# Kernel tuning notes

Measured on AMD Instinct MI355X. Metric: run time of the kernel, lower is better.

## Reference

```python
import jax, jax.numpy as jnp
import numpy as np


def setup_inputs() -> dict:
    key = jax.random.key(0)
    ks = jax.random.split(key, 8)
    N, E, H, C, L, G = 100000, 1600000, 128, 10, 5, 64
    x = jax.random.normal(ks[0], (N, H), dtype=jnp.float32)
    edge_index = jax.random.randint(ks[1], (2, E), 0, N, dtype=jnp.int32)
    batch = jnp.sort(jax.random.randint(ks[2], (N,), 0, G, dtype=jnp.int32))
    # Glorot-ish init scale for stability
    Ws = jax.random.normal(ks[3], (L, H, H), dtype=jnp.float32) * (1.0 / np.sqrt(H))
    bs = jax.random.normal(ks[4], (L, H), dtype=jnp.float32) * 0.01
    W_out = jax.random.normal(ks[5], (H, C), dtype=jnp.float32) * (1.0 / np.sqrt(H))
    b_out = jax.random.normal(ks[6], (C,), dtype=jnp.float32) * 0.01
    return {"x": x, "edge_index": edge_index, "batch": batch, "num_graphs": G,
            "Ws": Ws, "bs": bs, "W_out": W_out, "b_out": b_out}


def reference(x, edge_index, batch, num_graphs, Ws, bs, W_out, b_out):
    N = x.shape[0]
    # --- GCN normalization (add self-loops, symmetric deg^-1/2 norm), computed once ---
    loop = jnp.arange(N, dtype=edge_index.dtype)
    src = jnp.concatenate([edge_index[0], loop])  # message sources (x_j)
    dst = jnp.concatenate([edge_index[1], loop])  # aggregation targets
    deg = jax.ops.segment_sum(jnp.ones_like(dst, dtype=x.dtype), dst, num_segments=N)
    dis = jnp.where(deg > 0, jax.lax.rsqrt(jnp.maximum(deg, 1.0)), 0.0)
    norm = dis[src] * dis[dst]  # [E+N]
    # --- stacked GCNConv + ReLU ---
    for l in range(Ws.shape[0]):
        xw = x @ Ws[l]                                   # [N, H] dense transform
        msg = norm[:, None] * xw[src]                    # gather + scale per edge
        x = jax.nn.relu(jax.ops.segment_sum(msg, dst, num_segments=N) + bs[l])
    # --- global mean pool over graphs ---
    sums = jax.ops.segment_sum(x, batch, num_segments=num_graphs)       # [G, H]
    cnts = jax.ops.segment_sum(jnp.ones((N,), x.dtype), batch, num_segments=num_graphs)
    pooled = sums / jnp.maximum(cnts, 1.0)[:, None]
    return pooled @ W_out + b_out
```

## Files before the change

kernel.cpp:

```cpp
#include <hip/hip_runtime.h>
#include <hip/hip_bf16.h>
#include <stdint.h>

#define HDIM 128
#define SBITS 8
#define SBMASK 255
#define SBMAX 512

typedef __attribute__((ext_vector_type(8))) short short8;
typedef __attribute__((ext_vector_type(4))) float f32x4;
typedef __attribute__((ext_vector_type(2))) float f32x2;

__device__ __forceinline__ ushort f2bf(float f) {
  uint u = __float_as_uint(f);
  u = (u + 0x7fffu + ((u >> 16) & 1u)) >> 16;
  return (ushort)u;
}
__device__ __forceinline__ float bflo(uint v) { return __uint_as_float(v << 16); }
__device__ __forceinline__ float bfhi(uint v) { return __uint_as_float(v & 0xffff0000u); }

__device__ __forceinline__ int pdeg4(int c) { return (c + 4) & ~3; }

__device__ __forceinline__ uint pack_cw(int src, float w) {
  uint w15 = (__float_as_uint(w) + 0x8000u) >> 16;
  return (uint)src | (w15 << 17);
}
__device__ __forceinline__ uint cw_src(uint u) { return u & 0x1FFFFu; }
__device__ __forceinline__ float cw_w(uint u) { return __uint_as_float((u >> 17) << 16); }


__global__ __launch_bounds__(256) void bucket_edges(const int* __restrict__ ei,
                                                    int* __restrict__ bktcur,
                                                    uint* __restrict__ bkt, int E,
                                                    int cap) {
  __shared__ int hist[SBMAX], base[SBMAX];
  const int t = threadIdx.x;
  const int c0 = blockIdx.x * 2048;
  for (int i = t; i < SBMAX; i += 256) hist[i] = 0;
  __syncthreads();
  uint pk[8];
  int sb_[8], rk[8];
#pragma unroll
  for (int j = 0; j < 8; ++j) {
    int idx = c0 + j * 256 + t;
    sb_[j] = -1;
    if (idx < E) {
      int s = ei[idx];
      int d = ei[E + idx];
      int b = d >> SBITS;
      pk[j] = (uint)(d & SBMASK) | ((uint)s << SBITS);
      sb_[j] = b;
      rk[j] = atomicAdd(&hist[b], 1);
    }
  }
  __syncthreads();
  for (int i = t; i < SBMAX; i += 256)
    base[i] = hist[i] ? atomicAdd(&bktcur[i * 16], hist[i]) : 0;
  __syncthreads();
#pragma unroll
  for (int j = 0; j < 8; ++j)
    if (sb_[j] >= 0)
      bkt[(size_t)sb_[j] * cap + base[sb_[j]] + rk[j]] = pk[j];
}

__global__ __launch_bounds__(256) void csr_count(const uint* __restrict__ bkt,
                                                 const int* __restrict__ bktcur,
                                                 float* __restrict__ dis,
                                                 int* __restrict__ degs,
                                                 int* __restrict__ sbtot, int cap,
                                                 int N) {
  __shared__ int cnt[256];
  __shared__ int red[256];
  const int sb = blockIdx.x, t = threadIdx.x;
  const int n0 = sb << SBITS;
  const int ecnt = bktcur[sb * 16];
  const uint* eb = bkt + (size_t)sb * cap;
  cnt[t] = 0;
  __syncthreads();
  for (int i = t; i < ecnt; i += 256)
    atomicAdd(&cnt[__builtin_nontemporal_load(eb + i) & SBMASK], 1);
  __syncthreads();
  int s = 0;
  const int n = n0 + t;
  if (n < N) {
    int c = cnt[t];
    degs[n] = c;
    dis[n] = rsqrtf((float)(c + 1));
    s = pdeg4(c);
  }
  red[t] = s;
  __syncthreads();
  for (int off = 128; off; off >>= 1) {
    if (t < off) red[t] += red[t + off];
    __syncthreads();
  }
  if (t == 0) sbtot[sb] = red[0];
}

__global__ __launch_bounds__(512) void scan_sb(const int* __restrict__ sbtot,
                                               int* __restrict__ sbbase,
                                               int* __restrict__ rowptr, int SB,
                                               int N) {
  __shared__ int sh[SBMAX];
  int t = threadIdx.x;
  int v = (t < SB) ? sbtot[t] : 0;
  sh[t] = v;
  __syncthreads();
  for (int off = 1; off < SBMAX; off <<= 1) {
    int add = (t >= off) ? sh[t - off] : 0;
    __syncthreads();
    sh[t] += add;
    __syncthreads();
  }
  if (t < SB) sbbase[t] = sh[t] - v;
  if (t == SBMAX - 1) rowptr[N] = sh[SBMAX - 1];
}

__global__ __launch_bounds__(256) void csr_place(const uint* __restrict__ bkt,
                                                 const int* __restrict__ bktcur,
                                                 const int* __restrict__ sbbase,
                                                 const float* __restrict__ dis,
                                                 const int* __restrict__ degs,
                                                 int* __restrict__ rowptr,
                                                 uint* __restrict__ colw, int cap,
                                                 int N) {
  __shared__ int cur[256];
  __shared__ int sh[256];
  const int sb = blockIdx.x, t = threadIdx.x;
  const int n0 = sb << SBITS;
  const int ecnt = bktcur[sb * 16];
  const uint* eb = bkt + (size_t)sb * cap;
  const int base = sbbase[sb];
  const int n = n0 + t;
  const int deg = (n < N) ? degs[n] : 0;
  const int v = (n < N) ? pdeg4(deg) : 0;
  sh[t] = v;
  __syncthreads();
  for (int off = 1; off < 256; off <<= 1) {
    int add = (t >= off) ? sh[t - off] : 0;
    __syncthreads();
    sh[t] += add;
    __syncthreads();
  }
  const int p = sh[t] - v;
  if (n < N) {
    rowptr[n] = base + p;
    cur[t] = p + 1;
    float dn = dis[n];
    colw[base + p] = pack_cw(n, dn * dn);
    for (int q = deg + 1; q < v; ++q) colw[base + p + q] = (uint)n;
  }
  __syncthreads();
  for (int i = t; i < ecnt; i += 256) {
    uint u = __builtin_nontemporal_load(eb + i);
    int dloc = (int)(u & SBMASK);
    int s2 = (int)(u >> SBITS);
    int pos = atomicAdd(&cur[dloc], 1);
    int d = n0 + dloc;
    colw[base + pos] = pack_cw(s2, dis[s2] * dis[d]);
  }
}

__global__ __launch_bounds__(256) void swz_w(const float* __restrict__ Ws,
                                             ushort* __restrict__ Wsw, int total) {
  int idx = blockIdx.x * 256 + threadIdx.x;
  if (idx >= total) return;
  int l = idx >> 14, r = idx & 16383;
  int j = r & 7, lane = (r >> 3) & 63, kk = (r >> 9) & 3, c = r >> 11;
  int n = c * 16 + (lane & 15);
  int k = kk * 32 + (lane >> 4) * 8 + j;
  Wsw[idx] = f2bf(Ws[l * 16384 + k * HDIM + n]);
}


template <bool F32IN>
__global__ __launch_bounds__(256) void gemm_kernel(const void* __restrict__ Xin,
                                                   const ushort* __restrict__ Wsw,
                                                   ushort* __restrict__ XW, int N,
                                                   int ntiles) {
  __shared__ ushort wlds[16384];
  __shared__ ushort clds[64 * 136];
  const int t = threadIdx.x;
  {
    const int4* src = (const int4*)Wsw;
    int4* dst = (int4*)wlds;
#pragma unroll
    for (int i = 0; i < 8; ++i) dst[t + 256 * i] = src[t + 256 * i];
  }
  __syncthreads();

  const int wave = t >> 6, lane = t & 63;
  const int kq = lane >> 4;

  for (int tile = blockIdx.x; tile < ntiles; tile += gridDim.x) {
    const int row0 = tile * 64 + wave * 16 + (lane & 15);
    const bool inb = row0 < N;

    short8 afr[4];
#pragma unroll
    for (int kk = 0; kk < 4; ++kk) afr[kk] = short8{0, 0, 0, 0, 0, 0, 0, 0};
    if (inb) {
      if constexpr (F32IN) {
        const float* arow = (const float*)Xin + (size_t)row0 * HDIM;
#pragma unroll
        for (int kk = 0; kk < 4; ++kk) {
          float4 x0 = *(const float4*)(arow + kk * 32 + kq * 8);
          float4 x1 = *(const float4*)(arow + kk * 32 + kq * 8 + 4);
          short8 f;
          f[0] = (short)f2bf(x0.x); f[1] = (short)f2bf(x0.y);
          f[2] = (short)f2bf(x0.z); f[3] = (short)f2bf(x0.w);
          f[4] = (short)f2bf(x1.x); f[5] = (short)f2bf(x1.y);
          f[6] = (short)f2bf(x1.z); f[7] = (short)f2bf(x1.w);
          afr[kk] = f;
        }
      } else {
        const short8* arow = (const short8*)((const ushort*)Xin + (size_t)row0 * HDIM);
#pragma unroll
        for (int kk = 0; kk < 4; ++kk) afr[kk] = arow[kk * 4 + kq];
      }
    }

    f32x4 acc[8];
#pragma unroll
    for (int c = 0; c < 8; ++c) acc[c] = f32x4{0.f, 0.f, 0.f, 0.f};
#pragma unroll
    for (int kk = 0; kk < 4; ++kk) {
#pragma unroll
      for (int c = 0; c < 8; ++c) {
        short8 bfr = *(const short8*)(wlds + (((c * 4 + kk) * 64 + lane) << 3));
        acc[c] = __builtin_amdgcn_mfma_f32_16x16x32_bf16(afr[kk], bfr, acc[c], 0, 0, 0);
      }
    }

    __syncthreads();
    const int m0 = wave * 16 + kq * 4;
#pragma unroll
    for (int c = 0; c < 8; ++c) {
      int col = c * 16 + (lane & 15);
#pragma unroll
      for (int r = 0; r < 4; ++r) clds[(m0 + r) * 136 + col] = f2bf(acc[c][r]);
    }
    __syncthreads();
#pragma unroll
    for (int i = 0; i < 4; ++i) {
      int idx = t + 256 * i;
      int row = idx >> 4, piece = idx & 15;
      int grow = tile * 64 + row;
      if (grow < N)
        ((int4*)XW)[(size_t)tile * 1024 + idx] =
            *(const int4*)(clds + row * 136 + piece * 8);
    }
  }
}


template <int K, bool CLAMP>
__device__ __forceinline__ void agg_bulk(const ushort* __restrict__ XW,
                                         const uint* __restrict__ colw, int beg,
                                         int pdeg, int e, int c, f32x2* acc) {
  const int last = pdeg - 1;
  uint cw[K];
#pragma unroll
  for (int k = 0; k < K; ++k) {
    int off = 4 * k + e;
    if (CLAMP) off = off < pdeg ? off : last;
    cw[k] = __builtin_nontemporal_load(colw + beg + off);
  }
  uint4 gv[K];
#pragma unroll
  for (int k = 0; k < K; ++k)
    gv[k] = *(const uint4*)(XW + ((size_t)cw_src(cw[k]) << 7) + c * 8);
#pragma unroll
  for (int k = 0; k < K; ++k) {
    float w;
    if (CLAMP) {
      int off = 4 * k + e;
      w = (off < pdeg) ? cw_w(cw[k]) : 0.f;
    } else {
      w = cw_w(cw[k]);
    }
    f32x2 wv = f32x2{w, w};
    uint4 v = gv[k];
    acc[0] = __builtin_elementwise_fma(wv, f32x2{bflo(v.x), bfhi(v.x)}, acc[0]);
    acc[1] = __builtin_elementwise_fma(wv, f32x2{bflo(v.y), bfhi(v.y)}, acc[1]);
    acc[2] = __builtin_elementwise_fma(wv, f32x2{bflo(v.z), bfhi(v.z)}, acc[2]);
    acc[3] = __builtin_elementwise_fma(wv, f32x2{bflo(v.w), bfhi(v.w)}, acc[3]);
  }
}

__global__ __launch_bounds__(256, 3) void agg_kernel(const ushort* __restrict__ XW,
                                                     const uint* __restrict__ colw,
                                                     const int* __restrict__ rowptr,
                                                     const float* __restrict__ bias,
                                                     ushort* __restrict__ Y, int N) {
  const int lane = threadIdx.x & 63;
  const int node = blockIdx.x * 4 + (threadIdx.x >> 6);
  if (node >= N) return;
  const int e = lane >> 4, c = lane & 15;
  const int beg = rowptr[node];
  const int pdeg = rowptr[node + 1] - beg;
  const int nb = pdeg >> 2;

  f32x2 acc[4];
#pragma unroll
  for (int i = 0; i < 4; ++i) acc[i] = f32x2{0.f, 0.f};

  if (nb == 4) {
    agg_bulk<4, false>(XW, colw, beg, pdeg, e, c, acc);
  } else if (nb == 5) {
    agg_bulk<5, false>(XW, colw, beg, pdeg, e, c, acc);
  } else if (nb >= 6) {
    agg_bulk<6, false>(XW, colw, beg, pdeg, e, c, acc);
    for (int off = 24 + e; off < pdeg; off += 4) {
      uint u = __builtin_nontemporal_load(colw + beg + off);
      uint4 v = *(const uint4*)(XW + ((size_t)cw_src(u) << 7) + c * 8);
      float w = cw_w(u);
      f32x2 wv = f32x2{w, w};
      acc[0] = __builtin_elementwise_fma(wv, f32x2{bflo(v.x), bfhi(v.x)}, acc[0]);
      acc[1] = __builtin_elementwise_fma(wv, f32x2{bflo(v.y), bfhi(v.y)}, acc[1]);
      acc[2] = __builtin_elementwise_fma(wv, f32x2{bflo(v.z), bfhi(v.z)}, acc[2]);
      acc[3] = __builtin_elementwise_fma(wv, f32x2{bflo(v.w), bfhi(v.w)}, acc[3]);
    }
  } else {
    agg_bulk<4, true>(XW, colw, beg, pdeg, e, c, acc);
  }

#pragma unroll
  for (int i = 0; i < 4; ++i) {
    acc[i].x += __shfl_xor(acc[i].x, 16, 64);
    acc[i].y += __shfl_xor(acc[i].y, 16, 64);
    acc[i].x += __shfl_xor(acc[i].x, 32, 64);
    acc[i].y += __shfl_xor(acc[i].y, 32, 64);
  }
  if (e == 0) {
    float4 b0 = *(const float4*)(bias + c * 8);
    float4 b1 = *(const float4*)(bias + c * 8 + 4);
    uint4 pk;
    pk.x = (uint)f2bf(fmaxf(acc[0].x + b0.x, 0.f)) | ((uint)f2bf(fmaxf(acc[0].y + b0.y, 0.f)) << 16);
    pk.y = (uint)f2bf(fmaxf(acc[1].x + b0.z, 0.f)) | ((uint)f2bf(fmaxf(acc[1].y + b0.w, 0.f)) << 16);
    pk.z = (uint)f2bf(fmaxf(acc[2].x + b1.x, 0.f)) | ((uint)f2bf(fmaxf(acc[2].y + b1.y, 0.f)) << 16);
    pk.w = (uint)f2bf(fmaxf(acc[3].x + b1.z, 0.f)) | ((uint)f2bf(fmaxf(acc[3].y + b1.w, 0.f)) << 16);
    *(uint4*)(Y + (size_t)node * HDIM + c * 8) = pk;
  }
}


__global__ __launch_bounds__(256) void pool_partial(const ushort* __restrict__ x,
                                                    const int* __restrict__ batch,
                                                    float* __restrict__ pooled,
                                                    int* __restrict__ gcnt, int N) {
  const int g = blockIdx.x, s = blockIdx.y;
  const int t = threadIdx.x;
  __shared__ int range[2];
  __shared__ float sums[256];
  if (t < 2) {
    int target = g + t;
    int lo = 0, hi = N;
    while (lo < hi) {
      int mid = (lo + hi) >> 1;
      if (batch[mid] < target) lo = mid + 1;
      else hi = mid;
    }
    range[t] = lo;
  }
  __syncthreads();
  int beg = range[0], end = range[1];
  if (s == 0 && t == 0) gcnt[g] = end - beg;
  int col = t & 127, half = t >> 7;
  float acc = 0.f;
  for (int n = beg + s * 2 + half; n < end; n += 16) {
    acc += __uint_as_float(((uint)x[(size_t)n * HDIM + col]) << 16);
  }
  sums[t] = acc;
  __syncthreads();
  if (t < 128) atomicAdd(&pooled[g * HDIM + t], sums[t] + sums[t + 128]);
}

__global__ __launch_bounds__(256) void out_final(const float* __restrict__ pooled,
                                                 const int* __restrict__ gcnt,
                                                 const float* __restrict__ W_out,
                                                 const float* __restrict__ b_out,
                                                 float* __restrict__ out, int G, int C) {
  int i = blockIdx.x * 256 + threadIdx.x;
  if (i >= G * C) return;
  int g = i / C, c = i - g * C;
  float inv = 1.f / (float)max(gcnt[g], 1);
  const float* pg = pooled + g * HDIM;
  float o = 0.f;
  for (int h = 0; h < HDIM; ++h) o += pg[h] * W_out[h * C + c];
  out[i] = b_out[c] + o * inv;
}


extern "C" void kernel_launch(void* const* d_in, const int* in_sizes, int n_in,
                              void* d_out, int out_size, void* d_ws, size_t ws_size,
                              hipStream_t stream) {
  (void)n_in;
  (void)ws_size;
  const float* x = (const float*)d_in[0];
  const int* ei = (const int*)d_in[1];
  const int* batch = (const int*)d_in[2];
  const float* Ws = (const float*)d_in[4];
  const float* bs = (const float*)d_in[5];
  const float* W_out = (const float*)d_in[6];
  const float* b_out = (const float*)d_in[7];
  float* out = (float*)d_out;

  const int N = in_sizes[0] / HDIM;
  const int E = in_sizes[1] / 2;
  const int L = in_sizes[5] / HDIM;
  const int C = in_sizes[7];
  const int G = out_size / C;
  const int SB = (N + SBMASK) >> SBITS;
  const int cap = E / SB + 2048;

  char* p = (char*)d_ws;
  auto carve = [&](size_t bytes) {
    char* r = p;
    p += (bytes + 255) & ~(size_t)255;
    return r;
  };
  int* bktcur = (int*)carve(SBMAX * 64);
  float* dis = (float*)carve((size_t)N * 4);
  int* degs = (int*)carve((size_t)N * 4);
  int* rowptr = (int*)carve((size_t)(N + 1) * 4);
  int* sbtot = (int*)carve(SBMAX * 4);
  int* sbbase = (int*)carve(SBMAX * 4);
  uint* bkt = (uint*)carve((size_t)SB * cap * 4);
  uint* colw = (uint*)carve(((size_t)E + 4 * (size_t)N + 64) * 4);
  ushort* Wsw = (ushort*)carve((size_t)L * HDIM * HDIM * 2);
  ushort* xw = (ushort*)carve((size_t)N * HDIM * 2);
  ushort* y0 = (ushort*)carve((size_t)N * HDIM * 2);
  ushort* y1 = (ushort*)carve((size_t)N * HDIM * 2);
  float* pooled = (float*)carve((size_t)G * HDIM * 4 + (size_t)G * 4);
  int* gcnt = (int*)(pooled + (size_t)G * HDIM);

  hipMemsetAsync(bktcur, 0, SBMAX * 64, stream);
  hipMemsetAsync(pooled, 0, (size_t)G * HDIM * 4 + (size_t)G * 4, stream);

  bucket_edges<<<(E + 2047) / 2048, 256, 0, stream>>>(ei, bktcur, bkt, E, cap);
  csr_count<<<SB, 256, 0, stream>>>(bkt, bktcur, dis, degs, sbtot, cap, N);
  scan_sb<<<1, SBMAX, 0, stream>>>(sbtot, sbbase, rowptr, SB, N);
  csr_place<<<SB, 256, 0, stream>>>(bkt, bktcur, sbbase, dis, degs, rowptr, colw, cap, N);
  swz_w<<<(L * HDIM * HDIM + 255) / 256, 256, 0, stream>>>(Ws, Wsw, L * HDIM * HDIM);

  const int ntiles = (N + 63) / 64;
  const int gb = 768;
  gemm_kernel<true><<<gb, 256, 0, stream>>>(x, Wsw, xw, N, ntiles);
  agg_kernel<<<(N + 3) / 4, 256, 0, stream>>>(xw, colw, rowptr, bs, y0, N);
  ushort* xc = y0;
  ushort* xn = y1;
  for (int l = 1; l < L; ++l) {
    gemm_kernel<false><<<gb, 256, 0, stream>>>(xc, Wsw + (size_t)l * HDIM * HDIM, xw, N, ntiles);
    agg_kernel<<<(N + 3) / 4, 256, 0, stream>>>(xw, colw, rowptr, bs + (size_t)l * HDIM, xn, N);
    ushort* tmp = xc;
    xc = xn;
    xn = tmp;
  }
  pool_partial<<<dim3(G, 8), 256, 0, stream>>>(xc, batch, pooled, gcnt, N);
  out_final<<<(G * C + 255) / 256, 256, 0, stream>>>(pooled, gcnt, W_out, b_out, out, G, C);
}
```

Before: 542.6 us.

## Fuse mean-pool into final aggregation layer and move graph counts to scan

The last GCN aggregation layer now adds its ReLU outputs straight into the pooled per-graph sums through shared memory and atomics, so the final feature map is never written to global memory and the separate pool_partial kernel is dropped. Per-graph node counts are computed by binary search inside the scan_sb kernel instead. This saves a 25 MB bf16 write and re-read plus one launch, but adds global float atomics (usually one per feature column per block when all four nodes share a graph) and a __syncthreads in the last layer. Pooling also now sums fp32 values rather than bf16-rounded ones.

Result: no change. 545.0 us (+0.4%).

```diff
diff --git a/kernel.cpp b/kernel.cpp
--- a/kernel.cpp
+++ b/kernel.cpp
@@ -100,7 +100,8 @@
 __global__ __launch_bounds__(512) void scan_sb(const int* __restrict__ sbtot,
                                                int* __restrict__ sbbase,
                                                int* __restrict__ rowptr, int SB,
-                                               int N) {
+                                               int N, const int* __restrict__ batch,
+                                               int* __restrict__ gcnt, int G) {
   __shared__ int sh[SBMAX];
   int t = threadIdx.x;
   int v = (t < SB) ? sbtot[t] : 0;
@@ -114,6 +115,14 @@
   }
   if (t < SB) sbbase[t] = sh[t] - v;
   if (t == SBMAX - 1) rowptr[N] = sh[SBMAX - 1];
+  if (t < G) {
+    int lo = 0, hi = N;
+    while (lo < hi) { int m = (lo + hi) >> 1; if (batch[m] < t) lo = m + 1; else hi = m; }
+    int b0 = lo;
+    lo = 0; hi = N;
+    while (lo < hi) { int m = (lo + hi) >> 1; if (batch[m] < t + 1) lo = m + 1; else hi = m; }
+    gcnt[t] = lo - b0;
+  }
 }
 
 __global__ __launch_bounds__(256) void csr_place(const uint* __restrict__ bkt,
@@ -288,93 +297,104 @@
   }
 }
 
+template <bool POOL>
 __global__ __launch_bounds__(256, 3) void agg_kernel(const ushort* __restrict__ XW,
                                                      const uint* __restrict__ colw,
                                                      const int* __restrict__ rowptr,
                                                      const float* __restrict__ bias,
-                                                     ushort* __restrict__ Y, int N) {
+                                                     ushort* __restrict__ Y, int N,
+                                                     const int* __restrict__ batch,
+                                                     float* __restrict__ pooled) {
   const int lane = threadIdx.x & 63;
-  const int node = blockIdx.x * 4 + (threadIdx.x >> 6);
-  if (node >= N) return;
+  const int wave = threadIdx.x >> 6;
+  const int node = blockIdx.x * 4 + wave;
+  const bool valid = node < N;
+  if (!POOL && !valid) return;
   const int e = lane >> 4, c = lane & 15;
-  const int beg = rowptr[node];
-  const int pdeg = rowptr[node + 1] - beg;
-  const int nb = pdeg >> 2;
 
   f32x2 acc[4];
 #pragma unroll
   for (int i = 0; i < 4; ++i) acc[i] = f32x2{0.f, 0.f};
 
-  if (nb == 4) {
-    agg_bulk<4, false>(XW, colw, beg, pdeg, e, c, acc);
-  } else if (nb == 5) {
-    agg_bulk<5, false>(XW, colw, beg, pdeg, e, c, acc);
-  } else if (nb >= 6) {
-    agg_bulk<6, false>(XW, colw, beg, pdeg, e, c, acc);
-    for (int off = 24 + e; off < pdeg; off += 4) {
-      uint u = __builtin_nontemporal_load(colw + beg + off);
-      uint4 v = *(const uint4*)(XW + ((size_t)cw_src(u) << 7) + c * 8);
-      float w = cw_w(u);
-      f32x2 wv = f32x2{w, w};
-      acc[0] = __builtin_elementwise_fma(wv, f32x2{bflo(v.x), bfhi(v.x)}, acc[0]);
-      acc[1] = __builtin_elementwise_fma(wv, f32x2{bflo(v.y), bfhi(v.y)}, acc[1]);
-      acc[2] = __builtin_elementwise_fma(wv, f32x2{bflo(v.z), bfhi(v.z)}, acc[2]);
-      acc[3] = __builtin_elementwise_fma(wv, f32x2{bflo(v.w), bfhi(v.w)}, acc[3]);
+  if (valid) {
+    const int beg = rowptr[node];
+    const int pdeg = rowptr[node + 1] - beg;
+    const int nb = pdeg >> 2;
+
+    if (nb == 4) {
+      agg_bulk<4, false>(XW, colw, beg, pdeg, e, c, acc);
+    } else if (nb == 5) {
+      agg_bulk<5, false>(XW, colw, beg, pdeg, e, c, acc);
+    } else if (nb >= 6) {
+      agg_bulk<6, false>(XW, colw, beg, pdeg, e, c, acc);
+      for (int off = 24 + e; off < pdeg; off += 4) {
+        uint u = __builtin_nontemporal_load(colw + beg + off);
+        uint4 v = *(const uint4*)(XW + ((size_t)cw_src(u) << 7) + c * 8);
+        float w = cw_w(u);
+        f32x2 wv = f32x2{w, w};
+        acc[0] = __builtin_elementwise_fma(wv, f32x2{bflo(v.x), bfhi(v.x)}, acc[0]);
+        acc[1] = __builtin_elementwise_fma(wv, f32x2{bflo(v.y), bfhi(v.y)}, acc[1]);
+        acc[2] = __builtin_elementwise_fma(wv, f32x2{bflo(v.z), bfhi(v.z)}, acc[2]);
+        acc[3] = __builtin_elementwise_fma(wv, f32x2{bflo(v.w), bfhi(v.w)}, acc[3]);
+      }
+    } else {
+      agg_bulk<4, true>(XW, colw, beg, pdeg, e, c, acc);
+    }
+
+#pragma unroll
+    for (int i = 0; i < 4; ++i) {
+      acc[i].x += __shfl_xor(acc[i].x, 16, 64);
+      acc[i].y += __shfl_xor(acc[i].y, 16, 64);
+      acc[i].x += __shfl_xor(acc[i].x, 32, 64);
+      acc[i].y += __shfl_xor(acc[i].y, 32, 64);
+    }
+  }
+
+  if constexpr (!POOL) {
+    if (e == 0) {
+      float4 b0 = *(const float4*)(bias + c * 8);
+      float4 b1 = *(const float4*)(bias + c * 8 + 4);
+      uint4 pk;
+      pk.x = (uint)f2bf(fmaxf(acc[0].x + b0.x, 0.f)) | ((uint)f2bf(fmaxf(acc[0].y + b0.y, 0.f)) << 16);
+      pk.y = (uint)f2bf(fmaxf(acc[1].x + b0.z, 0.f)) | ((uint)f2bf(fmaxf(acc[1].y + b0.w, 0.f)) << 16);
+      pk.z = (uint)f2bf(fmaxf(acc[2].x + b1.x, 0.f)) | ((uint)f2bf(fmaxf(acc[2].y + b1.y, 0.f)) << 16);
+      pk.w = (uint)f2bf(fmaxf(acc[3].x + b1.z, 0.f)) | ((uint)f2bf(fmaxf(acc[3].y + b1.w, 0.f)) << 16);
+      *(uint4*)(Y + (size_t)node * HDIM + c * 8) = pk;
     }
   } else {
-    agg_bulk<4, true>(XW, colw, beg, pdeg, e, c, acc);
-  }
-
-#pragma unroll
-  for (int i = 0; i < 4; ++i) {
-    acc[i].x += __shfl_xor(acc[i].x, 16, 64);
-    acc[i].y += __shfl_xor(acc[i].y, 16, 64);
-    acc[i].x += __shfl_xor(acc[i].x, 32, 64);
-    acc[i].y += __shfl_xor(acc[i].y, 32, 64);
-  }
-  if (e == 0) {
-    float4 b0 = *(const float4*)(bias + c * 8);
-    float4 b1 = *(const float4*)(bias + c * 8 + 4);
-    uint4 pk;
-    pk.x = (uint)f2bf(fmaxf(acc[0].x + b0.x, 0.f)) | ((uint)f2bf(fmaxf(acc[0].y + b0.y, 0.f)) << 16);
-    pk.y = (uint)f2bf(fmaxf(acc[1].x + b0.z, 0.f)) | ((uint)f2bf(fmaxf(acc[1].y + b0.w, 0.f)) << 16);
-    pk.z = (uint)f2bf(fmaxf(acc[2].x + b1.x, 0.f)) | ((uint)f2bf(fmaxf(acc[2].y + b1.y, 0.f)) << 16);
-    pk.w = (uint)f2bf(fmaxf(acc[3].x + b1.z, 0.f)) | ((uint)f2bf(fmaxf(acc[3].y + b1.w, 0.f)) << 16);
-    *(uint4*)(Y + (size_t)node * HDIM + c * 8) = pk;
-  }
-}
-
-
-__global__ __launch_bounds__(256) void pool_partial(const ushort* __restrict__ x,
-                                                    const int* __restrict__ batch,
-                                                    float* __restrict__ pooled,
-                                                    int* __restrict__ gcnt, int N) {
-  const int g = blockIdx.x, s = blockIdx.y;
-  const int t = threadIdx.x;
-  __shared__ int range[2];
-  __shared__ float sums[256];
-  if (t < 2) {
-    int target = g + t;
-    int lo = 0, hi = N;
-    while (lo < hi) {
-      int mid = (lo + hi) >> 1;
-      if (batch[mid] < target) lo = mid + 1;
-      else hi = mid;
-    }
-    range[t] = lo;
-  }
-  __syncthreads();
-  int beg = range[0], end = range[1];
-  if (s == 0 && t == 0) gcnt[g] = end - beg;
-  int col = t & 127, half = t >> 7;
-  float acc = 0.f;
-  for (int n = beg + s * 2 + half; n < end; n += 16) {
-    acc += __uint_as_float(((uint)x[(size_t)n * HDIM + col]) << 16);
-  }
-  sums[t] = acc;
-  __syncthreads();
-  if (t < 128) atomicAdd(&pooled[g * HDIM + t], sums[t] + sums[t + 128]);
-}
+    __shared__ float psh[4][HDIM];
+    __shared__ int gsh[4];
+    if (valid && e == 0) {
+      float4 b0 = *(const float4*)(bias + c * 8);
+      float4 b1 = *(const float4*)(bias + c * 8 + 4);
+      float* row = &psh[wave][c * 8];
+      row[0] = fmaxf(acc[0].x + b0.x, 0.f);
+      row[1] = fmaxf(acc[0].y + b0.y, 0.f);
+      row[2] = fmaxf(acc[1].x + b0.z, 0.f);
+      row[3] = fmaxf(acc[1].y + b0.w, 0.f);
+      row[4] = fmaxf(acc[2].x + b1.x, 0.f);
+      row[5] = fmaxf(acc[2].y + b1.y, 0.f);
+      row[6] = fmaxf(acc[3].x + b1.z, 0.f);
+      row[7] = fmaxf(acc[3].y + b1.w, 0.f);
+    }
+    if (lane == 0) gsh[wave] = valid ? batch[node] : -1;
+    __syncthreads();
+    const int t = threadIdx.x;
+    if (t < HDIM) {
+      int g0 = gsh[0];
+      bool same = (g0 >= 0) & (gsh[1] == g0) & (gsh[2] == g0) & (gsh[3] == g0);
+      if (same) {
+        atomicAdd(&pooled[g0 * HDIM + t],
+                  psh[0][t] + psh[1][t] + psh[2][t] + psh[3][t]);
+      } else {
+#pragma unroll
+        for (int w = 0; w < 4; ++w)
+          if (gsh[w] >= 0) atomicAdd(&pooled[gsh[w] * HDIM + t], psh[w][t]);
+      }
+    }
+  }
+}
+
 
 __global__ __launch_bounds__(256) void out_final(const float* __restrict__ pooled,
                                                  const int* __restrict__ gcnt,
@@ -436,27 +456,33 @@
   int* gcnt = (int*)(pooled + (size_t)G * HDIM);
 
   hipMemsetAsync(bktcur, 0, SBMAX * 64, stream);
-  hipMemsetAsync(pooled, 0, (size_t)G * HDIM * 4 + (size_t)G * 4, stream);
+  hipMemsetAsync(pooled, 0, (size_t)G * HDIM * 4, stream);
 
   bucket_edges<<<(E + 2047) / 2048, 256, 0, stream>>>(ei, bktcur, bkt, E, cap);
   csr_count<<<SB, 256, 0, stream>>>(bkt, bktcur, dis, degs, sbtot, cap, N);
-  scan_sb<<<1, SBMAX, 0, stream>>>(sbtot, sbbase, rowptr, SB, N);
+  scan_sb<<<1, SBMAX, 0, stream>>>(sbtot, sbbase, rowptr, SB, N, batch, gcnt, G);
   csr_place<<<SB, 256, 0, stream>>>(bkt, bktcur, sbbase, dis, degs, rowptr, colw, cap, N);
   swz_w<<<(L * HDIM * HDIM + 255) / 256, 256, 0, stream>>>(Ws, Wsw, L * HDIM * HDIM);
 
   const int ntiles = (N + 63) / 64;
   const int gb = 768;
+  const int ab = (N + 3) / 4;
   gemm_kernel<true><<<gb, 256, 0, stream>>>(x, Wsw, xw, N, ntiles);
-  agg_kernel<<<(N + 3) / 4, 256, 0, stream>>>(xw, colw, rowptr, bs, y0, N);
+  agg_kernel<false><<<ab, 256, 0, stream>>>(xw, colw, rowptr, bs, y0, N, batch, pooled);
   ushort* xc = y0;
   ushort* xn = y1;
   for (int l = 1; l < L; ++l) {
     gemm_kernel<false><<<gb, 256, 0, stream>>>(xc, Wsw + (size_t)l * HDIM * HDIM, xw, N, ntiles);
-    agg_kernel<<<(N + 3) / 4, 256, 0, stream>>>(xw, colw, rowptr, bs + (size_t)l * HDIM, xn, N);
-    ushort* tmp = xc;
-    xc = xn;
-    xn = tmp;
-  }
-  pool_partial<<<dim3(G, 8), 256, 0, stream>>>(xc, batch, pooled, gcnt, N);
+    if (l < L - 1) {
+      agg_kernel<false><<<ab, 256, 0, stream>>>(xw, colw, rowptr, bs + (size_t)l * HDIM,
+                                                xn, N, batch, pooled);
+      ushort* tmp = xc;
+      xc = xn;
+      xn = tmp;
+    } else {
+      agg_kernel<true><<<ab, 256, 0, stream>>>(xw, colw, rowptr, bs + (size_t)l * HDIM,
+                                               nullptr, N, batch, pooled);
+    }
+  }
   out_final<<<(G * C + 255) / 256, 256, 0, stream>>>(pooled, gcnt, W_out, b_out, out, G, C);
 }
```
